# Performance work log

Measured on AMD Instinct MI355X. Metric: run time of the kernel, lower is better.

Reference implementation:

```python
import jax, jax.numpy as jnp
import numpy as np

B, L, D, H = 4, 2048, 1024, 16
DK = D // H  # 64


def setup_inputs() -> dict:
    key = jax.random.key(0)
    ks = jax.random.split(key, 5)
    x = jax.random.normal(ks[0], (B, L, D), dtype=jnp.float32)
    scale = 1.0 / np.sqrt(D)
    W_qkv = jax.random.normal(ks[1], (D, 3 * D), dtype=jnp.float32) * scale
    b_qkv = jnp.zeros((3 * D,), dtype=jnp.float32)
    W_out = jax.random.normal(ks[2], (D, D), dtype=jnp.float32) * scale
    b_out = jnp.zeros((D,), dtype=jnp.float32)
    return {"x": x, "W_qkv": W_qkv, "b_qkv": b_qkv, "W_out": W_out, "b_out": b_out}


def reference(x, W_qkv, b_qkv, W_out, b_out):
    Bx, Lx, Dx = x.shape
    qkv = x @ W_qkv + b_qkv                      # [B, L, 3D]
    q, k, v = jnp.split(qkv, 3, axis=-1)
    # [B, H, L, d_k]
    q = q.reshape(Bx, Lx, H, DK).transpose(0, 2, 1, 3)
    k = k.reshape(Bx, Lx, H, DK).transpose(0, 2, 1, 3)
    v = v.reshape(Bx, Lx, H, DK).transpose(0, 2, 1, 3)
    scores = jnp.einsum('bhqd,bhkd->bhqk', q, k) / np.sqrt(DK)
    causal = jnp.tril(jnp.ones((Lx, Lx), dtype=bool))
    scores = jnp.where(causal[None, None], scores, -jnp.inf)
    attn = jax.nn.softmax(scores, axis=-1)       # [B, H, L, L]
    out = jnp.einsum('bhqk,bhkd->bhqd', attn, v)
    out = out.transpose(0, 2, 1, 3).reshape(Bx, Lx, Dx)
    return out @ W_out + b_out
```

## Files before the change

### kernel.cpp

```cpp
#include <hip/hip_runtime.h>
#include <stdint.h>

#define B_ 4
#define L_ 2048
#define D_ 1024
#define H_ 16
#define DK_ 64

typedef __attribute__((ext_vector_type(8))) short bf16x8;
typedef __attribute__((ext_vector_type(4))) float f32x4;
typedef unsigned short bfu;

#define MFMA(a, b, c) __builtin_amdgcn_mfma_f32_16x16x32_bf16((a), (b), (c), 0, 0, 0)

__device__ __forceinline__ unsigned short f2bf(float f) {
  union { float f; unsigned int u; } v; v.f = f;
  unsigned int u = v.u;
  return (unsigned short)((u + 0x7fffu + ((u >> 16) & 1u)) >> 16);
}

__device__ __forceinline__ void gll16(const void* g, void* l) {
  __builtin_amdgcn_global_load_lds(
      (const __attribute__((address_space(1))) void*)g,
      (__attribute__((address_space(3))) void*)l, 16, 0, 0);
}

#define VMCNT(n_) asm volatile("s_waitcnt vmcnt(" #n_ ")" ::: "memory")
#define BARRIER() asm volatile("s_barrier" ::: "memory")


__global__ __launch_bounds__(256) void cast_x(const float* __restrict__ in,
                                              bfu* __restrict__ out, int n4) {
  int i = blockIdx.x * 256 + threadIdx.x;
  if (i >= n4) return;
  float4 v = ((const float4*)in)[i];
  ushort4 o;
  o.x = f2bf(v.x); o.y = f2bf(v.y); o.z = f2bf(v.z); o.w = f2bf(v.w);
  ((ushort4*)out)[i] = o;
}

__global__ __launch_bounds__(256) void wpack(const float* __restrict__ in,
                                             bfu* __restrict__ out, int K, int C) {
  int idx = blockIdx.x * 256 + threadIdx.x;
  if (idx >= K * C) return;
  int k = idx / C, c = idx % C;
  size_t o = ((size_t)(c >> 4) * (K >> 3) + (k >> 3)) * 128 + (c & 15) * 8 + (k & 7);
  out[o] = f2bf(in[idx]);
}


template <int EPI>
__global__ __launch_bounds__(256, 2) void gemm_r(
    const bfu* __restrict__ A, const bfu* __restrict__ Bp,
    const float* __restrict__ bias, bfu* __restrict__ Qg, bfu* __restrict__ Kg,
    bfu* __restrict__ Vtg, float* __restrict__ Out, int M, int N, int K) {
  __shared__ __align__(16) bfu As[2][128 * 64];
  const int tid = threadIdx.x;
  const int lane = tid & 63;
  const int w = tid >> 6;
  const int wm = w >> 1, wn = w & 1;
  const int l15 = lane & 15, l4 = lane >> 4;

  const int nwg = gridDim.x;
  const int cpx = nwg >> 3;
  const int bid = (int)blockIdx.x;
  const int swz = (bid & 7) * cpx + (bid >> 3);
  const int NTt = N / 128;
  const int m0 = ((swz & 7) + 8 * (swz / (8 * NTt))) * 128;
  const int n0 = ((swz >> 3) % NTt) * 128;
  const int K8 = K >> 3;

  auto stageA = [&](int t) {
    char* lb = (char*)As[t & 1];
#pragma unroll
    for (int j = 0; j < 4; ++j) {
      int idx = j * 256 + tid;
      int row = idx >> 3, c16p = idx & 7, c16 = c16p ^ (row & 7);
      gll16(A + (size_t)(m0 + row) * K + t * 64 + c16 * 8,
            lb + row * 128 + c16p * 16);
    }
  };

  const size_t bbase = ((size_t)((n0 + wn * 64) >> 4)) * K8;
  auto loadB = [&](int t, bf16x8 (&br)[4][2]) {
#pragma unroll
    for (int ni = 0; ni < 4; ++ni)
#pragma unroll
      for (int kk = 0; kk < 2; ++kk)
        br[ni][kk] = *(const bf16x8*)(
            Bp + (bbase + (size_t)ni * K8 + t * 8 + kk * 4 + l4) * 128 + l15 * 8);
  };

  f32x4 acc[4][4] = {};
  bf16x8 af[4][2], brA[4][2], brB[4][2];

  auto lda = [&](int t) {
    const char* base = (const char*)As[t & 1];
#pragma unroll
    for (int mi = 0; mi < 4; ++mi)
#pragma unroll
      for (int kk = 0; kk < 2; ++kk) {
        int row = wm * 64 + mi * 16 + l15;
        int ch = (kk * 4 + l4) ^ (row & 7);
        af[mi][kk] = *(const bf16x8*)(base + row * 128 + ch * 16);
      }
  };
  auto mm_all = [&](bf16x8 (&br)[4][2]) {
    __builtin_amdgcn_s_setprio(1);
#pragma unroll
    for (int kk = 0; kk < 2; ++kk)
#pragma unroll
      for (int mi = 0; mi < 4; ++mi)
#pragma unroll
        for (int ni = 0; ni < 4; ++ni)
          acc[mi][ni] = MFMA(af[mi][kk], br[ni][kk], acc[mi][ni]);
    __builtin_amdgcn_s_setprio(0);
  };

  const int NT = K >> 6;
  stageA(0);
  __builtin_amdgcn_sched_barrier(0);
  loadB(0, brA);
  loadB(1, brB);

  for (int t = 0; t < NT; t += 2) {
    VMCNT(8); BARRIER();
    lda(t);
    stageA(t + 1);
    __builtin_amdgcn_sched_barrier(0);
    mm_all(brA);
    if (t + 2 < NT) loadB(t + 2, brA);
    if (t + 2 < NT) { VMCNT(8); } else { VMCNT(0); }
    BARRIER();
    lda(t + 1);
    if (t + 2 < NT) stageA(t + 2);
    __builtin_amdgcn_sched_barrier(0);
    mm_all(brB);
    if (t + 3 < NT) loadB(t + 3, brB);
  }

  if constexpr (EPI == 1) {
#pragma unroll
    for (int ni = 0; ni < 4; ++ni) {
      int gn = n0 + wn * 64 + ni * 16 + l15;
      float bv = bias[gn];
#pragma unroll
      for (int mi = 0; mi < 4; ++mi)
#pragma unroll
        for (int rg = 0; rg < 4; ++rg) {
          int gm = m0 + wm * 64 + mi * 16 + l4 * 4 + rg;
          Out[(size_t)gm * N + gn] = acc[mi][ni][rg] + bv;
        }
    }
  } else {
    const int sec = n0 >> 10;
    if (sec < 2) {
      bfu* dst = (sec == 0) ? Qg : Kg;
      const float scale = (sec == 0) ? 0.18033688011112042f : 1.0f;
#pragma unroll
      for (int ni = 0; ni < 4; ++ni) {
        int gn = n0 + wn * 64 + ni * 16 + l15;
        int rem = gn & 1023;
        int hh = rem >> 6, dk = rem & 63;
        float bv = bias[gn];
#pragma unroll
        for (int mi = 0; mi < 4; ++mi)
#pragma unroll
          for (int rg = 0; rg < 4; ++rg) {
            int gm = m0 + wm * 64 + mi * 16 + l4 * 4 + rg;
            int bb = gm >> 11, ll = gm & 2047;
            dst[(((size_t)(bb * H_ + hh)) * L_ + ll) * DK_ + dk] =
                f2bf((acc[mi][ni][rg] + bv) * scale);
          }
      }
    } else {
      __syncthreads();
#pragma unroll
      for (int ni = 0; ni < 4; ++ni) {
        int n_local = wn * 64 + ni * 16 + l15;
        int gn = n0 + n_local;
        float bv = bias[gn];
        int swzn = (n_local & 7) << 4;
#pragma unroll
        for (int mi = 0; mi < 4; ++mi) {
          int m_base = wm * 64 + mi * 16 + l4 * 4;
          int k6 = m_base & 63;
          int p0 = (m_base & ~63) |
                   ((k6 & 32) | (((k6 >> 2) & 3) << 3) | (((k6 >> 4) & 1) << 2));
          float v0 = acc[mi][ni][0] + bv, v1 = acc[mi][ni][1] + bv;
          float v2 = acc[mi][ni][2] + bv, v3 = acc[mi][ni][3] + bv;
          uint32_t w01, w23;
          asm("v_cvt_pk_bf16_f32 %0, %1, %2" : "=v"(w01) : "v"(v0), "v"(v1));
          asm("v_cvt_pk_bf16_f32 %0, %1, %2" : "=v"(w23) : "v"(v2), "v"(v3));
          *(uint32_t*)((char*)As + n_local * 256 + ((2 * p0) ^ swzn)) = w01;
          *(uint32_t*)((char*)As + n_local * 256 + ((2 * p0 + 4) ^ swzn)) = w23;
        }
      }
      __syncthreads();
      int n = tid >> 1;
      int cb = (tid & 1) * 8;
      int gnn = n0 + n;
      int hh = (gnn >> 6) & 15, dk = gnn & 63;
      size_t rowbase =
          (((size_t)((m0 >> 11) * H_ + hh)) * DK_ + dk) * L_ + (m0 & 2047);
#pragma unroll
      for (int j = 0; j < 8; ++j) {
        int ch = cb + j;
        bf16x8 vv = *(const bf16x8*)((char*)As + n * 256 +
                                     ((ch * 16) ^ ((n & 7) << 4)));
        *(bf16x8*)(Vtg + rowbase + ch * 8) = vv;
      }
    }
  }
}


__global__ __launch_bounds__(256, 3) void attn(const bfu* __restrict__ Qg,
                                               const bfu* __restrict__ Kg,
                                               const bfu* __restrict__ Vtg,
                                               bfu* __restrict__ Ao) {
  __shared__ __align__(16) bfu Ks[2 * 64 * 64];
  __shared__ __align__(16) bfu Vs[2 * 64 * 64];

  const int tid = threadIdx.x;
  const int lane = tid & 63;
  const int w = tid >> 6;
  const int l15 = lane & 15, l4 = lane >> 4;

  const int hid = blockIdx.x;
  const int xcd = hid & 7, slot = hid >> 3;
  const int bh = xcd * 8 + (slot >> 3);
  const int p = slot & 7;
  const int b = bh >> 4, h = bh & 15;

  for (int seg = 0; seg < 2; ++seg) {
    const int qb = (seg == 0) ? p : 15 - p;
    const int q0 = qb * 128;
    const int nt = 2 * qb + 2;
    const int q0w = q0 + w * 32;

    bf16x8 qf[2][2];
#pragma unroll
    for (int mi = 0; mi < 2; ++mi)
#pragma unroll
      for (int kk = 0; kk < 2; ++kk)
        qf[mi][kk] = *(const bf16x8*)(
            Qg + ((size_t)bh * L_ + q0w + mi * 16 + l15) * DK_ + kk * 32 + l4 * 8);

#pragma unroll
    for (int i = 0; i < 2; ++i) {
      int lb = i * 256 + tid;
      int r = lb >> 3, c16 = (lb & 7) ^ (r & 7);
      gll16(Kg + ((size_t)bh * L_ + r) * DK_ + c16 * 8, (char*)Ks + lb * 16);
      gll16(Vtg + ((size_t)bh * DK_ + r) * L_ + c16 * 8, (char*)Vs + lb * 16);
    }
    VMCNT(0);
    BARRIER();

    f32x4 acco[2][4] = {};
    float m[2] = {-1e30f, -1e30f};
    float l[2] = {0.f, 0.f};

    for (int t = 0; t < nt; ++t) {
      const int cur = t & 1;
      const int kv0 = t * 64;
      const char* Kc = (const char*)Ks + cur * 8192;
      const char* Vc = (const char*)Vs + cur * 8192;

      if (t + 1 < nt) {
        const int nb = (t + 1) & 1, nkv = (t + 1) * 64;
#pragma unroll
        for (int i = 0; i < 2; ++i) {
          int lb = i * 256 + tid;
          int r = lb >> 3, c16 = (lb & 7) ^ (r & 7);
          gll16(Kg + ((size_t)bh * L_ + nkv + r) * DK_ + c16 * 8,
                (char*)Ks + nb * 8192 + lb * 16);
          gll16(Vtg + ((size_t)bh * DK_ + r) * L_ + nkv + c16 * 8,
                (char*)Vs + nb * 8192 + lb * 16);
        }
        VMCNT(4);
      } else {
        VMCNT(0);
      }
      BARRIER();

      if (kv0 <= q0w + 31) {
        f32x4 s[2][4] = {};
        __builtin_amdgcn_s_setprio(1);
#pragma unroll
        for (int kk = 0; kk < 2; ++kk)
#pragma unroll
          for (int ni = 0; ni < 4; ++ni) {
            int r = ni * 16 + l15;
            int ch = (kk * 4 + l4) ^ (r & 7);
            bf16x8 kf = *(const bf16x8*)(Kc + r * 128 + ch * 16);
#pragma unroll
            for (int mi = 0; mi < 2; ++mi)
              s[mi][ni] = MFMA(kf, qf[mi][kk], s[mi][ni]);
          }
        __builtin_amdgcn_s_setprio(0);

        if (kv0 + 63 > q0w) {
#pragma unroll
          for (int mi = 0; mi < 2; ++mi) {
            int qg_ = q0w + mi * 16 + l15;
#pragma unroll
            for (int ni = 0; ni < 4; ++ni) {
              int kvg = kv0 + ni * 16 + l4 * 4;
#pragma unroll
              for (int rg = 0; rg < 4; ++rg)
                if (kvg + rg > qg_) s[mi][ni][rg] = -1e30f;
            }
          }
        }

        float mx[2];
#pragma unroll
        for (int mi = 0; mi < 2; ++mi) {
          float v = fmaxf(fmaxf(fmaxf(s[mi][0][0], s[mi][0][1]),
                                fmaxf(s[mi][0][2], s[mi][0][3])),
                          fmaxf(fmaxf(s[mi][1][0], s[mi][1][1]),
                                fmaxf(s[mi][1][2], s[mi][1][3])));
          v = fmaxf(v, fmaxf(fmaxf(fmaxf(s[mi][2][0], s[mi][2][1]),
                                   fmaxf(s[mi][2][2], s[mi][2][3])),
                             fmaxf(fmaxf(s[mi][3][0], s[mi][3][1]),
                                   fmaxf(s[mi][3][2], s[mi][3][3]))));
          v = fmaxf(v, __shfl_xor(v, 16));
          v = fmaxf(v, __shfl_xor(v, 32));
          mx[mi] = v;
        }
        float grow = fmaxf(mx[0] - m[0], mx[1] - m[1]);
        if (__any(grow > 11.0f)) {
#pragma unroll
          for (int mi = 0; mi < 2; ++mi) {
            float mn = fmaxf(m[mi], mx[mi]);
            float sc = __builtin_amdgcn_exp2f(m[mi] - mn);
            m[mi] = mn;
            l[mi] *= sc;
#pragma unroll
            for (int rg = 0; rg < 4; ++rg) {
              float scq = __shfl(sc, l4 * 4 + rg);
              acco[mi][0][rg] *= scq; acco[mi][1][rg] *= scq;
              acco[mi][2][rg] *= scq; acco[mi][3][rg] *= scq;
            }
          }
        }

        uint32_t pk[2][4][2];
#pragma unroll
        for (int mi = 0; mi < 2; ++mi)
#pragma unroll
          for (int ni = 0; ni < 4; ++ni) {
            float p0 = __builtin_amdgcn_exp2f(s[mi][ni][0] - m[mi]);
            float p1 = __builtin_amdgcn_exp2f(s[mi][ni][1] - m[mi]);
            float p2 = __builtin_amdgcn_exp2f(s[mi][ni][2] - m[mi]);
            float p3 = __builtin_amdgcn_exp2f(s[mi][ni][3] - m[mi]);
            l[mi] += (p0 + p1) + (p2 + p3);
            asm("v_cvt_pk_bf16_f32 %0, %1, %2" : "=v"(pk[mi][ni][0]) : "v"(p0), "v"(p1));
            asm("v_cvt_pk_bf16_f32 %0, %1, %2" : "=v"(pk[mi][ni][1]) : "v"(p2), "v"(p3));
          }

        __builtin_amdgcn_s_setprio(1);
#pragma unroll
        for (int kk = 0; kk < 2; ++kk) {
          union { uint32_t wd[4]; bf16x8 v; } u[2];
#pragma unroll
          for (int mi = 0; mi < 2; ++mi) {
            u[mi].wd[0] = pk[mi][2 * kk][0];
            u[mi].wd[1] = pk[mi][2 * kk][1];
            u[mi].wd[2] = pk[mi][2 * kk + 1][0];
            u[mi].wd[3] = pk[mi][2 * kk + 1][1];
          }
#pragma unroll
          for (int ni = 0; ni < 4; ++ni) {
            int r = ni * 16 + l15;
            int ch = (kk * 4 + l4) ^ (r & 7);
            bf16x8 vf = *(const bf16x8*)(Vc + r * 128 + ch * 16);
#pragma unroll
            for (int mi = 0; mi < 2; ++mi)
              acco[mi][ni] = MFMA(u[mi].v, vf, acco[mi][ni]);
          }
        }
        __builtin_amdgcn_s_setprio(0);
      }

      BARRIER();
    }

#pragma unroll
    for (int mi = 0; mi < 2; ++mi) {
      float ls = l[mi];
      ls += __shfl_xor(ls, 16);
      ls += __shfl_xor(ls, 32);
      float linv = 1.0f / ls;
#pragma unroll
      for (int rg = 0; rg < 4; ++rg) {
        float lq = __shfl(linv, l4 * 4 + rg);
        int q = q0w + mi * 16 + l4 * 4 + rg;
#pragma unroll
        for (int ni = 0; ni < 4; ++ni) {
          int d = ni * 16 + l15;
          Ao[((size_t)b * L_ + q) * D_ + h * DK_ + d] = f2bf(acco[mi][ni][rg] * lq);
        }
      }
    }
  }
}


extern "C" void kernel_launch(void* const* d_in, const int* in_sizes, int n_in,
                              void* d_out, int out_size, void* d_ws, size_t ws_size,
                              hipStream_t stream) {
  const float* x = (const float*)d_in[0];
  const float* W_qkv = (const float*)d_in[1];
  const float* b_qkv = (const float*)d_in[2];
  const float* W_out = (const float*)d_in[3];
  const float* b_out = (const float*)d_in[4];
  float* out = (float*)d_out;

  char* ws = (char*)d_ws;
  bfu* xb     = (bfu*)(ws);
  bfu* Wqkv_p = (bfu*)(ws + 16777216);
  bfu* Wout_p = (bfu*)(ws + 23068672);
  bfu* Qg     = (bfu*)(ws + 25165824);
  bfu* Kg     = (bfu*)(ws + 41943040);
  bfu* Vtg    = (bfu*)(ws + 58720256);
  bfu* Ao     = (bfu*)(ws + 75497472);

  cast_x<<<8192, 256, 0, stream>>>(x, xb, 2097152);
  wpack<<<12288, 256, 0, stream>>>(W_qkv, Wqkv_p, 1024, 3072);
  wpack<<<4096, 256, 0, stream>>>(W_out, Wout_p, 1024, 1024);

  gemm_r<0><<<1536, 256, 0, stream>>>(xb, Wqkv_p, b_qkv, Qg, Kg, Vtg, nullptr,
                                      8192, 3072, 1024);
  attn<<<512, 256, 0, stream>>>(Qg, Kg, Vtg, Ao);
  gemm_r<1><<<512, 256, 0, stream>>>(Ao, Wout_p, b_out, nullptr, nullptr, nullptr,
                                     out, 8192, 1024, 1024);
}
```

Baseline: 163.9 us.

## Triple-buffer attention K/V staging and vectorize weight packing kernel

The attention kernel moves from a double to a triple LDS ring for K/V tiles, prefetching two tiles ahead with adjusted vmcnt waits to hide global-load latency better. The weight pack kernel now has each thread convert eight consecutive k values and write them as two vector stores, which cuts thread count and scattered 2-byte writes. The max reduction is also regrouped. The triple buffer raises LDS per block to 48KB, which may reduce occupancy below the launch bound of 3 blocks.

```diff
diff --git a/kernel.cpp b/kernel.cpp
--- a/kernel.cpp
+++ b/kernel.cpp
@@ -39,13 +39,17 @@
   ((ushort4*)out)[i] = o;
 }
 
-__global__ __launch_bounds__(256) void wpack(const float* __restrict__ in,
-                                             bfu* __restrict__ out, int K, int C) {
+__global__ __launch_bounds__(256) void wpack2(const float* __restrict__ in,
+                                              bfu* __restrict__ out, int K, int C) {
   int idx = blockIdx.x * 256 + threadIdx.x;
-  if (idx >= K * C) return;
-  int k = idx / C, c = idx % C;
-  size_t o = ((size_t)(c >> 4) * (K >> 3) + (k >> 3)) * 128 + (c & 15) * 8 + (k & 7);
-  out[o] = f2bf(in[idx]);
+  int c = idx % C, kb = idx / C;
+  if (kb >= (K >> 3)) return;
+  unsigned short v[8];
+#pragma unroll
+  for (int j = 0; j < 8; ++j) v[j] = f2bf(in[(size_t)(kb * 8 + j) * C + c]);
+  size_t o = ((size_t)(c >> 4) * (K >> 3) + kb) * 128 + (c & 15) * 8;
+  *(ushort4*)(out + o) = make_ushort4(v[0], v[1], v[2], v[3]);
+  *(ushort4*)(out + o + 4) = make_ushort4(v[4], v[5], v[6], v[7]);
 }
 
 
@@ -219,8 +223,8 @@
                                                const bfu* __restrict__ Kg,
                                                const bfu* __restrict__ Vtg,
                                                bfu* __restrict__ Ao) {
-  __shared__ __align__(16) bfu Ks[2 * 64 * 64];
-  __shared__ __align__(16) bfu Vs[2 * 64 * 64];
+  __shared__ __align__(16) bfu Ks[3 * 64 * 64];
+  __shared__ __align__(16) bfu Vs[3 * 64 * 64];
 
   const int tid = threadIdx.x;
   const int lane = tid & 63;
@@ -247,13 +251,22 @@
         qf[mi][kk] = *(const bf16x8*)(
             Qg + ((size_t)bh * L_ + q0w + mi * 16 + l15) * DK_ + kk * 32 + l4 * 8);
 
-#pragma unroll
-    for (int i = 0; i < 2; ++i) {
-      int lb = i * 256 + tid;
-      int r = lb >> 3, c16 = (lb & 7) ^ (r & 7);
-      gll16(Kg + ((size_t)bh * L_ + r) * DK_ + c16 * 8, (char*)Ks + lb * 16);
-      gll16(Vtg + ((size_t)bh * DK_ + r) * L_ + c16 * 8, (char*)Vs + lb * 16);
-    }
+    auto stageKV = [&](int tt) {
+      const int nb = tt % 3;
+      const int nkv = tt * 64;
+#pragma unroll
+      for (int i = 0; i < 2; ++i) {
+        int lb = i * 256 + tid;
+        int rr = lb >> 3, c16 = (lb & 7) ^ (rr & 7);
+        gll16(Kg + ((size_t)bh * L_ + nkv + rr) * DK_ + c16 * 8,
+              (char*)Ks + nb * 8192 + lb * 16);
+        gll16(Vtg + ((size_t)bh * DK_ + rr) * L_ + nkv + c16 * 8,
+              (char*)Vs + nb * 8192 + lb * 16);
+      }
+    };
+
+    stageKV(0);
+    stageKV(1);
     VMCNT(0);
     BARRIER();
 
@@ -262,22 +275,15 @@
     float l[2] = {0.f, 0.f};
 
     for (int t = 0; t < nt; ++t) {
-      const int cur = t & 1;
+      const int cur = t % 3;
       const int kv0 = t * 64;
       const char* Kc = (const char*)Ks + cur * 8192;
       const char* Vc = (const char*)Vs + cur * 8192;
 
-      if (t + 1 < nt) {
-        const int nb = (t + 1) & 1, nkv = (t + 1) * 64;
-#pragma unroll
-        for (int i = 0; i < 2; ++i) {
-          int lb = i * 256 + tid;
-          int r = lb >> 3, c16 = (lb & 7) ^ (r & 7);
-          gll16(Kg + ((size_t)bh * L_ + nkv + r) * DK_ + c16 * 8,
-                (char*)Ks + nb * 8192 + lb * 16);
-          gll16(Vtg + ((size_t)bh * DK_ + r) * L_ + nkv + c16 * 8,
-                (char*)Vs + nb * 8192 + lb * 16);
-        }
+      if (t + 2 < nt) {
+        stageKV(t + 2);
+        VMCNT(8);
+      } else if (t + 1 < nt) {
         VMCNT(4);
       } else {
         VMCNT(0);
@@ -291,9 +297,9 @@
         for (int kk = 0; kk < 2; ++kk)
 #pragma unroll
           for (int ni = 0; ni < 4; ++ni) {
-            int r = ni * 16 + l15;
-            int ch = (kk * 4 + l4) ^ (r & 7);
-            bf16x8 kf = *(const bf16x8*)(Kc + r * 128 + ch * 16);
+            int rr = ni * 16 + l15;
+            int ch = (kk * 4 + l4) ^ (rr & 7);
+            bf16x8 kf = *(const bf16x8*)(Kc + rr * 128 + ch * 16);
 #pragma unroll
             for (int mi = 0; mi < 2; ++mi)
               s[mi][ni] = MFMA(kf, qf[mi][kk], s[mi][ni]);
@@ -317,14 +323,13 @@
         float mx[2];
 #pragma unroll
         for (int mi = 0; mi < 2; ++mi) {
-          float v = fmaxf(fmaxf(fmaxf(s[mi][0][0], s[mi][0][1]),
-                                fmaxf(s[mi][0][2], s[mi][0][3])),
-                          fmaxf(fmaxf(s[mi][1][0], s[mi][1][1]),
-                                fmaxf(s[mi][1][2], s[mi][1][3])));
-          v = fmaxf(v, fmaxf(fmaxf(fmaxf(s[mi][2][0], s[mi][2][1]),
-                                   fmaxf(s[mi][2][2], s[mi][2][3])),
-                             fmaxf(fmaxf(s[mi][3][0], s[mi][3][1]),
-                                   fmaxf(s[mi][3][2], s[mi][3][3]))));
+          float t1 = fmaxf(fmaxf(s[mi][0][0], s[mi][0][1]), s[mi][0][2]);
+          float t2 = fmaxf(fmaxf(s[mi][0][3], s[mi][1][0]), s[mi][1][1]);
+          float t3 = fmaxf(fmaxf(s[mi][1][2], s[mi][1][3]), s[mi][2][0]);
+          float t4 = fmaxf(fmaxf(s[mi][2][1], s[mi][2][2]), s[mi][2][3]);
+          float t5 = fmaxf(fmaxf(s[mi][3][0], s[mi][3][1]), s[mi][3][2]);
+          float v = fmaxf(fmaxf(t1, t2), t3);
+          v = fmaxf(fmaxf(v, t4), fmaxf(t5, s[mi][3][3]));
           v = fmaxf(v, __shfl_xor(v, 16));
           v = fmaxf(v, __shfl_xor(v, 32));
           mx[mi] = v;
@@ -373,9 +378,9 @@
           }
 #pragma unroll
           for (int ni = 0; ni < 4; ++ni) {
-            int r = ni * 16 + l15;
-            int ch = (kk * 4 + l4) ^ (r & 7);
-            bf16x8 vf = *(const bf16x8*)(Vc + r * 128 + ch * 16);
+            int rr = ni * 16 + l15;
+            int ch = (kk * 4 + l4) ^ (rr & 7);
+            bf16x8 vf = *(const bf16x8*)(Vc + rr * 128 + ch * 16);
 #pragma unroll
             for (int mi = 0; mi < 2; ++mi)
               acco[mi][ni] = MFMA(u[mi].v, vf, acco[mi][ni]);
@@ -428,8 +433,8 @@
   bfu* Ao     = (bfu*)(ws + 75497472);
 
   cast_x<<<8192, 256, 0, stream>>>(x, xb, 2097152);
-  wpack<<<12288, 256, 0, stream>>>(W_qkv, Wqkv_p, 1024, 3072);
-  wpack<<<4096, 256, 0, stream>>>(W_out, Wout_p, 1024, 1024);
+  wpack2<<<1536, 256, 0, stream>>>(W_qkv, Wqkv_p, 1024, 3072);
+  wpack2<<<512, 256, 0, stream>>>(W_out, Wout_p, 1024, 1024);
 
   gemm_r<0><<<1536, 256, 0, stream>>>(xb, Wqkv_p, b_qkv, Qg, Kg, Vtg, nullptr,
                                       8192, 3072, 1024);
```

New measurement: 160.3 us (median of 2 runs). 1.02x faster.
